# Kernel tuning notes

Hardware: AMD Instinct MI355X
Metric: run time of the kernel (lower is better)

The kernel has to match this reference:

```python
import jax, jax.numpy as jnp
import numpy as np

B, T, C, H = 2, 2048, 1024, 16
HD = C // H  # head dim = 64


def setup_inputs() -> dict:
    key = jax.random.key(0)
    ks = jax.random.split(key, 12)
    s = 1.0 / np.sqrt(C)
    return {
        "q": jax.random.normal(ks[0], (B, T, C), jnp.float32),
        "k": jax.random.normal(ks[1], (B, T, C), jnp.float32),
        "v": jax.random.normal(ks[2], (B, T, C), jnp.float32),
        "attn_bias": jax.random.normal(ks[3], (1, H, T, T), jnp.float32),
        "Wq": jax.random.normal(ks[4], (C, C), jnp.float32) * s,
        "bq": jnp.zeros((C,), jnp.float32),
        "Wk": jax.random.normal(ks[5], (C, C), jnp.float32) * s,
        "bk": jnp.zeros((C,), jnp.float32),
        "Wv": jax.random.normal(ks[6], (C, C), jnp.float32) * s,
        "bv": jnp.zeros((C,), jnp.float32),
        "Wp": jax.random.normal(ks[7], (C, C), jnp.float32) * s,
        "bp": jnp.zeros((C,), jnp.float32),
    }


def reference(q, k, v, attn_bias, Wq, bq, Wk, bk, Wv, bv, Wp, bp):
    # Linear projections (torch Linear: x @ W.T + b), then split heads -> [B,H,T,HD]
    def split_heads(x):
        return x.reshape(B, T, H, HD).transpose(0, 2, 1, 3)

    qh = split_heads(q @ Wq.T + bq)
    kh = split_heads(k @ Wk.T + bk)
    vh = split_heads(v @ Wv.T + bv)

    scale = 1.0 / np.sqrt(HD)
    att = jnp.einsum("bhqd,bhkd->bhqk", qh, kh) * scale  # [B,H,T,T]

    causal = jnp.tril(jnp.ones((T, T), dtype=bool))  # mask[:, :, -Tq:, :Tk]
    att_scores = jnp.where(causal[None, None], att, -jnp.inf)
    att_scores = att_scores + attn_bias

    att_probs = jax.nn.softmax(att_scores, axis=-1)
    y = jnp.einsum("bhqk,bhkd->bhqd", att_probs, vh)
    y = y.transpose(0, 2, 1, 3).reshape(B, T, C)
    y = y @ Wp.T + bp  # dropout p=0.0
    return (y, att_scores)
```

## Files before the change

### kernel.cpp

```cpp
#include <hip/hip_runtime.h>
#include <hip/hip_bf16.h>
#include <math.h>

#define B_ 2
#define T_ 2048
#define C_ 1024
#define H_ 16
#define HD_ 64
#define M_ (B_*T_)
#define K_ 1024

#define SCORE_NINF (-3.0e38f)

#define PART_BH 33792

typedef __attribute__((ext_vector_type(8))) short bf16x8;
typedef __attribute__((ext_vector_type(8))) unsigned short u16x8;
typedef __attribute__((ext_vector_type(4))) float f32x4;

__device__ __forceinline__ ushort f2bf_rne(float x) {
    union { float f; unsigned u; } c; c.f = x;
    unsigned r = c.u + 0x7fffu + ((c.u >> 16) & 1u);
    return (ushort)(r >> 16);
}
__device__ __forceinline__ float bfval(ushort h) {
    union { float f; unsigned u; } c; c.u = ((unsigned)h) << 16; return c.f;
}
__device__ __forceinline__ ushort bf16_hi(float x) {
    union { float f; unsigned u; } c; c.f = x; return (ushort)(c.u >> 16);
}
__device__ __forceinline__ void nt_store_f4(float* p, f32x4 v) {
    __builtin_nontemporal_store(v, (f32x4*)p);
}

__device__ __forceinline__ void gload_lds16(const void* g, void* l) {
    __builtin_amdgcn_global_load_lds(
        (const __attribute__((address_space(1))) unsigned int*)g,
        (__attribute__((address_space(3))) unsigned int*)l, 16, 0, 0);
}

__global__ __launch_bounds__(256) void split_kernel(
    const float* __restrict__ src, ushort* __restrict__ hi,
    ushort* __restrict__ lo, int n)
{
    const int i = (blockIdx.x * 256 + threadIdx.x) * 4;
    if (i >= n) return;
    const float4 x = *(const float4*)&src[i];
    ushort4 h, l;
    h.x = f2bf_rne(x.x); l.x = f2bf_rne(x.x - bfval(h.x));
    h.y = f2bf_rne(x.y); l.y = f2bf_rne(x.y - bfval(h.y));
    h.z = f2bf_rne(x.z); l.z = f2bf_rne(x.z - bfval(h.z));
    h.w = f2bf_rne(x.w); l.w = f2bf_rne(x.w - bfval(h.w));
    *(ushort4*)&hi[i] = h;
    *(ushort4*)&lo[i] = l;
}

template<int MODE, int ASRC>
__global__ __launch_bounds__(256) void gemm_mfma(
    const float*  __restrict__ Xf,
    const ushort* __restrict__ Xh, const ushort* __restrict__ Xl,
    const ushort* __restrict__ Wh, const ushort* __restrict__ Wl,
    const float*  __restrict__ bias,
    float* __restrict__ outf, ushort* __restrict__ out_hi, ushort* __restrict__ out_lo)
{
    constexpr int APITCH = (ASRC == 0) ? 40 : 32;
    __shared__ ushort AhS[128 * APITCH];
    __shared__ ushort AlS[128 * APITCH];
    __shared__ ushort BhS[128 * 32];
    __shared__ ushort BlS[128 * 32];

    const int tid  = threadIdx.x;
    const int lane = tid & 63;
    const int w    = tid >> 6;
    const int lr   = lane & 15, lk = lane >> 4;
    const int wr   = w >> 1,    wc = w & 1;
    const int bm   = blockIdx.x * 128;
    const int bn   = blockIdx.y * 128;

    f32x4 acc[4][4];
    #pragma unroll
    for (int i = 0; i < 4; ++i)
        #pragma unroll
        for (int j = 0; j < 4; ++j) acc[i][j] = (f32x4){0.f, 0.f, 0.f, 0.f};

    const int ar   = tid >> 1;
    const int aseg = (tid & 1) * 16;

    for (int k0 = 0; k0 < K_; k0 += 32) {
        {
            const int r0 = w * 32;
            #pragma unroll
            for (int ii = 0; ii < 2; ++ii) {
                const int rr = r0 + ii * 16;
                const size_t goff = (size_t)(bn + rr + (lane >> 2)) * K_ + k0 + (lane & 3) * 8;
                gload_lds16(Wh + goff, &BhS[rr * 32]);
                gload_lds16(Wl + goff, &BlS[rr * 32]);
            }
            if constexpr (ASRC == 1) {
                #pragma unroll
                for (int ii = 0; ii < 2; ++ii) {
                    const int rr = r0 + ii * 16;
                    const size_t goff = (size_t)(bm + rr + (lane >> 2)) * K_ + k0 + (lane & 3) * 8;
                    gload_lds16(Xh + goff, &AhS[rr * 32]);
                    gload_lds16(Xl + goff, &AlS[rr * 32]);
                }
            }
        }
        if constexpr (ASRC == 0) {
            const float* xp = Xf + (size_t)(bm + ar) * K_ + aseg + k0;
            const float4 f0 = *(const float4*)(xp + 0);
            const float4 f1 = *(const float4*)(xp + 4);
            const float4 f2 = *(const float4*)(xp + 8);
            const float4 f3 = *(const float4*)(xp + 12);
            float xs[16];
            xs[0]=f0.x; xs[1]=f0.y; xs[2]=f0.z; xs[3]=f0.w;
            xs[4]=f1.x; xs[5]=f1.y; xs[6]=f1.z; xs[7]=f1.w;
            xs[8]=f2.x; xs[9]=f2.y; xs[10]=f2.z; xs[11]=f2.w;
            xs[12]=f3.x; xs[13]=f3.y; xs[14]=f3.z; xs[15]=f3.w;
            u16x8 hv[2], lv[2];
            #pragma unroll
            for (int e = 0; e < 16; ++e) {
                const ushort hh = f2bf_rne(xs[e]);
                const ushort ll = f2bf_rne(xs[e] - bfval(hh));
                hv[e >> 3][e & 7] = hh;
                lv[e >> 3][e & 7] = ll;
            }
            *(u16x8*)&AhS[ar * APITCH + aseg]     = hv[0];
            *(u16x8*)&AhS[ar * APITCH + aseg + 8] = hv[1];
            *(u16x8*)&AlS[ar * APITCH + aseg]     = lv[0];
            *(u16x8*)&AlS[ar * APITCH + aseg + 8] = lv[1];
        }
        __syncthreads();

        bf16x8 afr[4][2], bfr[4][2];
        #pragma unroll
        for (int i = 0; i < 4; ++i) {
            const int arow = wr * 64 + i * 16 + lr;
            afr[i][0] = *(const bf16x8*)&AhS[arow * APITCH + lk * 8];
            afr[i][1] = *(const bf16x8*)&AlS[arow * APITCH + lk * 8];
        }
        #pragma unroll
        for (int j = 0; j < 4; ++j) {
            const int brow = wc * 64 + j * 16 + lr;
            bfr[j][0] = *(const bf16x8*)&BhS[brow * 32 + lk * 8];
            bfr[j][1] = *(const bf16x8*)&BlS[brow * 32 + lk * 8];
        }
        #pragma unroll
        for (int i = 0; i < 4; ++i)
            #pragma unroll
            for (int j = 0; j < 4; ++j) {
                acc[i][j] = __builtin_amdgcn_mfma_f32_16x16x32_bf16(afr[i][0], bfr[j][0], acc[i][j], 0, 0, 0);
                acc[i][j] = __builtin_amdgcn_mfma_f32_16x16x32_bf16(afr[i][0], bfr[j][1], acc[i][j], 0, 0, 0);
                acc[i][j] = __builtin_amdgcn_mfma_f32_16x16x32_bf16(afr[i][1], bfr[j][0], acc[i][j], 0, 0, 0);
            }
        __syncthreads();
    }

    const int m0 = bm + wr * 64;
    const int n0 = bn + wc * 64;
    #pragma unroll
    for (int j = 0; j < 4; ++j) {
        const int n = n0 + j * 16 + lr;
        const float bias_n = bias[n];
        #pragma unroll
        for (int i = 0; i < 4; ++i) {
            if constexpr (MODE == 2) {
                const int mbase = m0 + i * 16 + lk * 4;
                const int bb = mbase >> 11, t0 = mbase & 2047;
                const int hh = n >> 6, dd = n & 63;
                ushort4 h4, l4;
                float o;
                o = acc[i][j][0] + bias_n; h4.x = f2bf_rne(o); l4.x = f2bf_rne(o - bfval(h4.x));
                o = acc[i][j][1] + bias_n; h4.y = f2bf_rne(o); l4.y = f2bf_rne(o - bfval(h4.y));
                o = acc[i][j][2] + bias_n; h4.z = f2bf_rne(o); l4.z = f2bf_rne(o - bfval(h4.z));
                o = acc[i][j][3] + bias_n; h4.w = f2bf_rne(o); l4.w = f2bf_rne(o - bfval(h4.w));
                const size_t base = (((size_t)(bb * H_ + hh)) * HD_ + dd) * T_ + t0;
                *(ushort4*)&out_hi[base] = h4;
                *(ushort4*)&out_lo[base] = l4;
            } else {
                #pragma unroll
                for (int q = 0; q < 4; ++q) {
                    const int m = m0 + i * 16 + lk * 4 + q;
                    const float o = acc[i][j][q] + bias_n;
                    if constexpr (MODE == 0) {
                        outf[(size_t)m * C_ + n] = o;
                    } else {
                        const int bb = m >> 11, tt = m & 2047;
                        const int hh = n >> 6, dd = n & 63;
                        const size_t idx = (((size_t)(bb * H_ + hh)) * T_ + tt) * HD_ + dd;
                        const ushort hv2 = f2bf_rne(o);
                        out_hi[idx] = hv2;
                        out_lo[idx] = f2bf_rne(o - bfval(hv2));
                    }
                }
            }
        }
    }
}

__global__ __launch_bounds__(256) void tail_kernel(float* __restrict__ scores)
{
    const int bh = blockIdx.y;
    const int r0 = blockIdx.x * 8;
    const int tid = threadIdx.x;
    const f32x4 ninf4 = (f32x4){SCORE_NINF, SCORE_NINF, SCORE_NINF, SCORE_NINF};
    #pragma unroll
    for (int rr = 0; rr < 8; ++rr) {
        float* row = scores + ((size_t)bh * T_ + r0 + rr) * T_ + 1024;
        nt_store_f4(row + tid * 4, ninf4);
    }
}

#define SPITCH 1028

__global__ __launch_bounds__(256) void score_kernel(
    const ushort* __restrict__ q_hi, const ushort* __restrict__ q_lo,
    const ushort* __restrict__ k_hi, const ushort* __restrict__ k_lo,
    const float* __restrict__ bias,
    float* __restrict__ scores, float2* __restrict__ partials)
{
    __shared__ float tile[16 * SPITCH];

    const int tid  = threadIdx.x;
    const int w    = tid >> 6, lane = tid & 63;
    const int lr   = lane & 15, lk = lane >> 4;

    const int bh = blockIdx.x / 192;
    const int r  = blockIdx.x - bh * 192;
    int s, j;
    if (r < 64) { s = r; j = 0; }
    else        { s = 64 + ((r - 64) >> 1); j = (r - 64) & 1; }
    const int h = bh & 15;
    const int qr0 = s * 16;
    const int cbase = j * 1024;
    const int ktmax = s >> 2;
    const int ktbase = j * 16;

    const ushort* qhb = q_hi + (size_t)bh * T_ * HD_;
    const ushort* qlb = q_lo + (size_t)bh * T_ * HD_;
    const ushort* khb = k_hi + (size_t)bh * T_ * HD_;
    const ushort* klb = k_lo + (size_t)bh * T_ * HD_;

    #pragma unroll
    for (int rr = 0; rr < 4; ++rr) {
        const int row = w * 4 + rr;
        const float* gsrc = bias + ((size_t)h * T_ + qr0 + row) * T_ + cbase + lane * 4;
        #pragma unroll
        for (int ch = 0; ch < 4; ++ch)
            gload_lds16(gsrc + ch * 256, &tile[row * SPITCH + ch * 256]);
    }
    __syncthreads();

    const int qrow = qr0 + lr;
    float2* part_bh = partials + (size_t)bh * PART_BH;
    bf16x8 qf[2][2];
    #pragma unroll
    for (int s2 = 0; s2 < 2; ++s2) {
        const size_t qoff = (size_t)qrow * HD_ + s2 * 32 + lk * 8;
        qf[s2][0] = *(const bf16x8*)&qhb[qoff];
        qf[s2][1] = *(const bf16x8*)&qlb[qoff];
    }
    const f32x4 ninf4 = (f32x4){SCORE_NINF, SCORE_NINF, SCORE_NINF, SCORE_NINF};

    #pragma unroll
    for (int i = 0; i < 4; ++i) {
        const int kt  = ktbase + w * 4 + i;
        const int lc0 = (kt - ktbase) * 64;
        if (kt > ktmax) {
            #pragma unroll
            for (int c = 0; c < 4; ++c)
                *(f32x4*)&tile[lr * SPITCH + lc0 + c * 16 + lk * 4] = ninf4;
            continue;
        }
        const int climit = (kt < ktmax) ? 4 : ((s & 3) + 1);
        f32x4 sc[4];
        #pragma unroll
        for (int c = 0; c < 4; ++c) {
            if (c < climit) {
                f32x4 a = (f32x4){0.f, 0.f, 0.f, 0.f};
                #pragma unroll
                for (int s2 = 0; s2 < 2; ++s2) {
                    const size_t koff = (size_t)(kt * 64 + c * 16 + lr) * HD_ + s2 * 32 + lk * 8;
                    const bf16x8 kfh = *(const bf16x8*)&khb[koff];
                    const bf16x8 kfl = *(const bf16x8*)&klb[koff];
                    a = __builtin_amdgcn_mfma_f32_16x16x32_bf16(kfh, qf[s2][0], a, 0, 0, 0);
                    a = __builtin_amdgcn_mfma_f32_16x16x32_bf16(kfl, qf[s2][0], a, 0, 0, 0);
                    a = __builtin_amdgcn_mfma_f32_16x16x32_bf16(kfh, qf[s2][1], a, 0, 0, 0);
                }
                sc[c] = a;
            }
        }
        float tmax = SCORE_NINF;
        #pragma unroll
        for (int c = 0; c < 4; ++c) {
            const int loff = lr * SPITCH + lc0 + c * 16 + lk * 4;
            if (c < climit) {
                const f32x4 b4 = *(const f32x4*)&tile[loff];
                f32x4 o;
                const int kc0 = kt * 64 + c * 16 + lk * 4;
                #pragma unroll
                for (int q4 = 0; q4 < 4; ++q4) {
                    const float sv = (kc0 + q4 <= qrow) ? sc[c][q4] * 0.125f + b4[q4]
                                                        : SCORE_NINF;
                    sc[c][q4] = sv;
                    tmax = fmaxf(tmax, sv);
                    o[q4] = sv;
                }
                *(f32x4*)&tile[loff] = o;
            } else {
                *(f32x4*)&tile[loff] = ninf4;
            }
        }
        tmax = fmaxf(tmax, __shfl_xor(tmax, 16));
        tmax = fmaxf(tmax, __shfl_xor(tmax, 32));
        float tsum = 0.f;
        #pragma unroll
        for (int c = 0; c < 4; ++c) {
            if (c < climit) {
                tsum += __expf(sc[c][0] - tmax);
                tsum += __expf(sc[c][1] - tmax);
                tsum += __expf(sc[c][2] - tmax);
                tsum += __expf(sc[c][3] - tmax);
            }
        }
        tsum += __shfl_xor(tsum, 16);
        tsum += __shfl_xor(tsum, 32);
        if (lk == 0)
            part_bh[kt * (2080 - 32 * kt) + (qrow - kt * 64)] = make_float2(tmax, tsum);
    }
    __syncthreads();

    #pragma unroll
    for (int row = 0; row < 16; ++row) {
        const f32x4 v = *(const f32x4*)&tile[row * SPITCH + tid * 4];
        *(f32x4*)&scores[((size_t)bh * T_ + qr0 + row) * T_ + cbase + tid * 4] = v;
    }
}

__global__ __launch_bounds__(256) void reduce_kernel(
    const float2* __restrict__ partials, float2* __restrict__ ml)
{
    const int gid = blockIdx.x * 256 + threadIdx.x;
    const int bh = gid >> 11, r = gid & 2047;
    const float2* pb = partials + (size_t)bh * PART_BH;
    const int nt = (r >> 6) + 1;
    float M = SCORE_NINF;
    for (int t = 0; t < nt; ++t)
        M = fmaxf(M, pb[t * (2080 - 32 * t) + (r - (t << 6))].x);
    float L = 0.f;
    for (int t = 0; t < nt; ++t) {
        const float2 p = pb[t * (2080 - 32 * t) + (r - (t << 6))];
        L += p.y * __expf(p.x - M);
    }
    ml[gid] = make_float2(M, 1.f / L);
}

#define PVPITCH 260

__global__ __launch_bounds__(256) void pv_kernel(
    const ushort* __restrict__ vt_hi, const ushort* __restrict__ vt_lo,
    const float* __restrict__ scores, const float2* __restrict__ ml,
    ushort* __restrict__ y_hi, ushort* __restrict__ y_lo)
{
    __shared__ float stile[16 * PVPITCH];

    const int tid = threadIdx.x;
    const int w = tid >> 6, lane = tid & 63;
    const int lr = lane & 15, lk = lane >> 4;
    const int bh = (int)blockIdx.x >> 6;
    const int p  = (int)blockIdx.x & 63;
    const int h = bh & 15, b = bh >> 4;

    const ushort* vhb = vt_hi + (size_t)bh * HD_ * T_;
    const ushort* vlb = vt_lo + (size_t)bh * HD_ * T_;

    #pragma unroll 1
    for (int half = 0; half < 2; ++half) {
        const int s = half ? (127 - p) : p;
        const int qr0 = s * 16;
        const int ktmax = s >> 2;
        const int nch = (ktmax + 4) >> 2;
        const float2 ml2 = ml[(size_t)bh * 2048 + qr0 + lr];
        const float M = ml2.x, invL = ml2.y;

        f32x4 yacc[4];
        #pragma unroll
        for (int c = 0; c < 4; ++c) yacc[c] = (f32x4){0.f, 0.f, 0.f, 0.f};

        #pragma unroll 1
        for (int ch = 0; ch < nch; ++ch) {
            const int cb = ch * 256;
            #pragma unroll
            for (int rr = 0; rr < 4; ++rr) {
                const int row = w * 4 + rr;
                const float* gsrc = scores + ((size_t)bh * T_ + qr0 + row) * T_ + cb + lane * 4;
                gload_lds16(gsrc, &stile[row * PVPITCH]);
            }
            __syncthreads();

            const int kt = ch * 4 + w;
            if (kt <= ktmax) {
                const int climit = (kt < ktmax) ? 4 : ((s & 3) + 1);
                const int s2max = (climit > 2) ? 2 : 1;
                bf16x8 pa[2][2];
                #pragma unroll
                for (int s2 = 0; s2 < 2; ++s2) {
                    if (s2 < s2max) {
                        const float* lsrc = &stile[lr * PVPITCH + w * 64 + s2 * 32 + lk * 8];
                        const f32x4 l0 = *(const f32x4*)(lsrc);
                        const f32x4 l1 = *(const f32x4*)(lsrc + 4);
                        float xs[8];
                        xs[0]=l0[0]; xs[1]=l0[1]; xs[2]=l0[2]; xs[3]=l0[3];
                        xs[4]=l1[0]; xs[5]=l1[1]; xs[6]=l1[2]; xs[7]=l1[3];
                        bf16x8 ph, pl;
                        #pragma unroll
                        for (int jj = 0; jj < 8; ++jj) {
                            const float pv = __expf(xs[jj] - M);
                            const ushort hv = bf16_hi(pv);
                            ph[jj] = (short)hv;
                            pl[jj] = (short)bf16_hi(pv - bfval(hv));
                        }
                        pa[s2][0] = ph;
                        pa[s2][1] = pl;
                    }
                }
                #pragma unroll
                for (int c2 = 0; c2 < 4; ++c2) {
                    #pragma unroll
                    for (int s2 = 0; s2 < 2; ++s2) {
                        if (s2 < s2max) {
                            const size_t voff = (size_t)(c2 * 16 + lr) * T_ + kt * 64 + s2 * 32 + lk * 8;
                            const bf16x8 vfh = *(const bf16x8*)&vhb[voff];
                            const bf16x8 vfl = *(const bf16x8*)&vlb[voff];
                            yacc[c2] = __builtin_amdgcn_mfma_f32_16x16x32_bf16(pa[s2][0], vfh, yacc[c2], 0, 0, 0);
                            yacc[c2] = __builtin_amdgcn_mfma_f32_16x16x32_bf16(pa[s2][0], vfl, yacc[c2], 0, 0, 0);
                            yacc[c2] = __builtin_amdgcn_mfma_f32_16x16x32_bf16(pa[s2][1], vfh, yacc[c2], 0, 0, 0);
                        }
                    }
                }
            }
            __syncthreads();
        }

        float* mbuf = stile;
        if (w > 0) {
            #pragma unroll
            for (int c2 = 0; c2 < 4; ++c2)
                *(f32x4*)&mbuf[((c2 * 3 + (w - 1)) * 64 + lane) * 4] = yacc[c2];
        }
        __syncthreads();
        if (w == 0) {
            float inv[4];
            #pragma unroll
            for (int q4 = 0; q4 < 4; ++q4) inv[q4] = __shfl(invL, lk * 4 + q4);
            #pragma unroll
            for (int c2 = 0; c2 < 4; ++c2) {
                f32x4 tot = yacc[c2];
                #pragma unroll
                for (int ww = 0; ww < 3; ++ww)
                    tot += *(const f32x4*)&mbuf[((c2 * 3 + ww) * 64 + lane) * 4];
                #pragma unroll
                for (int q4 = 0; q4 < 4; ++q4) {
                    const int yr = qr0 + lk * 4 + q4;
                    const float val = tot[q4] * inv[q4];
                    const size_t yi = ((size_t)b * T_ + yr) * C_ + h * HD_ + c2 * 16 + lr;
                    const ushort hv = f2bf_rne(val);
                    y_hi[yi] = hv;
                    y_lo[yi] = f2bf_rne(val - bfval(hv));
                }
            }
        }
        __syncthreads();
    }
}

extern "C" void kernel_launch(void* const* d_in, const int* in_sizes, int n_in,
                              void* d_out, int out_size, void* d_ws, size_t ws_size,
                              hipStream_t stream) {
    const float* q         = (const float*)d_in[0];
    const float* k         = (const float*)d_in[1];
    const float* v         = (const float*)d_in[2];
    const float* attn_bias = (const float*)d_in[3];
    const float* Wq        = (const float*)d_in[4];
    const float* bq        = (const float*)d_in[5];
    const float* Wk        = (const float*)d_in[6];
    const float* bk        = (const float*)d_in[7];
    const float* Wv        = (const float*)d_in[8];
    const float* bv        = (const float*)d_in[9];
    const float* Wp        = (const float*)d_in[10];
    const float* bp        = (const float*)d_in[11];

    float* y_out      = (float*)d_out;
    float* scores_out = y_out + (size_t)B_*T_*C_;

    ushort* ws = (ushort*)d_ws;
    const size_t NE = (size_t)B_*H_*T_*HD_;
    ushort* q_hi  = ws + 0*NE;
    ushort* q_lo  = ws + 1*NE;
    ushort* k_hi  = ws + 2*NE;
    ushort* k_lo  = ws + 3*NE;
    ushort* vt_hi = ws + 4*NE;
    ushort* vt_lo = ws + 5*NE;
    ushort* Wh1   = ws + 6*NE;
    ushort* Wl1   = Wh1 + (size_t)C_*K_;
    float2* partials = (float2*)(ws + 6*NE);
    float2* ml    = (float2*)(ws + 0*NE);
    ushort* y_hi  = ws + 6*NE;
    ushort* y_lo  = ws + 7*NE;
    ushort* Wph   = ws + 2*NE;
    ushort* Wpl   = ws + 3*NE;

    const dim3 gg(M_/128, C_/128);

    split_kernel<<<1024, 256, 0, stream>>>(Wq, Wh1, Wl1, C_*K_);
    gemm_mfma<1,0><<<gg, 256, 0, stream>>>(q, nullptr, nullptr, Wh1, Wl1, bq,
                                           nullptr, q_hi, q_lo);
    split_kernel<<<1024, 256, 0, stream>>>(Wk, Wh1, Wl1, C_*K_);
    gemm_mfma<1,0><<<gg, 256, 0, stream>>>(k, nullptr, nullptr, Wh1, Wl1, bk,
                                           nullptr, k_hi, k_lo);
    split_kernel<<<1024, 256, 0, stream>>>(Wv, Wh1, Wl1, C_*K_);
    gemm_mfma<2,0><<<gg, 256, 0, stream>>>(v, nullptr, nullptr, Wh1, Wl1, bv,
                                           nullptr, vt_hi, vt_lo);

    tail_kernel<<<dim3(128, 32), 256, 0, stream>>>(scores_out);
    score_kernel<<<6144, 256, 0, stream>>>(q_hi, q_lo, k_hi, k_lo, attn_bias,
                                           scores_out, partials);
    reduce_kernel<<<256, 256, 0, stream>>>(partials, ml);
    pv_kernel<<<2048, 256, 0, stream>>>(vt_hi, vt_lo, scores_out, ml, y_hi, y_lo);

    split_kernel<<<1024, 256, 0, stream>>>(Wp, Wph, Wpl, C_*K_);
    gemm_mfma<0,1><<<gg, 256, 0, stream>>>(nullptr, y_hi, y_lo, Wph, Wpl, bp,
                                           y_out, nullptr, nullptr);
}
```

Baseline: 715.2 us.

## Batch weight splits and QKV GEMMs into single launches, fold tail fill into score kernel

Replaces four separate weight hi/lo split launches with one split kernel covering all weights, and merges the three QKV projection GEMMs into one launch using blockIdx.z to select the input. The separate tail kernel that filled the upper half of score rows with -inf is removed, and that fill now happens inside the score kernel. The workspace layout is reshuffled so all split weights coexist, which needs more workspace and carries a risk of buffer aliasing between y, the partials and the q/k buffers.

```diff
diff --git a/kernel.cpp b/kernel.cpp
--- a/kernel.cpp
+++ b/kernel.cpp
@@ -39,12 +39,19 @@
         (__attribute__((address_space(3))) unsigned int*)l, 16, 0, 0);
 }
 
-__global__ __launch_bounds__(256) void split_kernel(
-    const float* __restrict__ src, ushort* __restrict__ hi,
-    ushort* __restrict__ lo, int n)
+__global__ __launch_bounds__(256) void split4_kernel(
+    const float* __restrict__ W0, const float* __restrict__ W1,
+    const float* __restrict__ W2, const float* __restrict__ W3,
+    ushort* __restrict__ h0, ushort* __restrict__ l0,
+    ushort* __restrict__ h1, ushort* __restrict__ l1,
+    ushort* __restrict__ h2, ushort* __restrict__ l2,
+    ushort* __restrict__ h3, ushort* __restrict__ l3)
 {
-    const int i = (blockIdx.x * 256 + threadIdx.x) * 4;
-    if (i >= n) return;
+    const int wsel = blockIdx.x >> 10;
+    const float* src = (wsel == 0) ? W0 : (wsel == 1) ? W1 : (wsel == 2) ? W2 : W3;
+    ushort* hi = (wsel == 0) ? h0 : (wsel == 1) ? h1 : (wsel == 2) ? h2 : h3;
+    ushort* lo = (wsel == 0) ? l0 : (wsel == 1) ? l1 : (wsel == 2) ? l2 : l3;
+    const int i = (((blockIdx.x & 1023) * 256) + threadIdx.x) * 4;
     const float4 x = *(const float4*)&src[i];
     ushort4 h, l;
     h.x = f2bf_rne(x.x); l.x = f2bf_rne(x.x - bfval(h.x));
@@ -55,19 +62,29 @@
     *(ushort4*)&lo[i] = l;
 }
 
-template<int MODE, int ASRC>
-__global__ __launch_bounds__(256) void gemm_mfma(
-    const float*  __restrict__ Xf,
-    const ushort* __restrict__ Xh, const ushort* __restrict__ Xl,
-    const ushort* __restrict__ Wh, const ushort* __restrict__ Wl,
-    const float*  __restrict__ bias,
-    float* __restrict__ outf, ushort* __restrict__ out_hi, ushort* __restrict__ out_lo)
+__global__ __launch_bounds__(256) void gemm_qkv(
+    const float* __restrict__ Xq, const float* __restrict__ Xk, const float* __restrict__ Xv,
+    const ushort* __restrict__ Wqh, const ushort* __restrict__ Wql,
+    const ushort* __restrict__ Wkh, const ushort* __restrict__ Wkl,
+    const ushort* __restrict__ Wvh, const ushort* __restrict__ Wvl,
+    const float* __restrict__ bq, const float* __restrict__ bk, const float* __restrict__ bv,
+    ushort* __restrict__ qo_hi, ushort* __restrict__ qo_lo,
+    ushort* __restrict__ ko_hi, ushort* __restrict__ ko_lo,
+    ushort* __restrict__ vo_hi, ushort* __restrict__ vo_lo)
 {
-    constexpr int APITCH = (ASRC == 0) ? 40 : 32;
+    constexpr int APITCH = 40;
     __shared__ ushort AhS[128 * APITCH];
     __shared__ ushort AlS[128 * APITCH];
     __shared__ ushort BhS[128 * 32];
     __shared__ ushort BlS[128 * 32];
+
+    const int z = blockIdx.z;
+    const float*  Xf = (z == 0) ? Xq : (z == 1) ? Xk : Xv;
+    const ushort* Wh = (z == 0) ? Wqh : (z == 1) ? Wkh : Wvh;
+    const ushort* Wl = (z == 0) ? Wql : (z == 1) ? Wkl : Wvl;
+    const float*  bias = (z == 0) ? bq : (z == 1) ? bk : bv;
+    ushort* out_hi = (z == 0) ? qo_hi : (z == 1) ? ko_hi : vo_hi;
+    ushort* out_lo = (z == 0) ? qo_lo : (z == 1) ? ko_lo : vo_lo;
 
     const int tid  = threadIdx.x;
     const int lane = tid & 63;
@@ -96,17 +113,8 @@
                 gload_lds16(Wh + goff, &BhS[rr * 32]);
                 gload_lds16(Wl + goff, &BlS[rr * 32]);
             }
-            if constexpr (ASRC == 1) {
-                #pragma unroll
-                for (int ii = 0; ii < 2; ++ii) {
-                    const int rr = r0 + ii * 16;
-                    const size_t goff = (size_t)(bm + rr + (lane >> 2)) * K_ + k0 + (lane & 3) * 8;
-                    gload_lds16(Xh + goff, &AhS[rr * 32]);
-                    gload_lds16(Xl + goff, &AlS[rr * 32]);
-                }
-            }
-        }
-        if constexpr (ASRC == 0) {
+        }
+        {
             const float* xp = Xf + (size_t)(bm + ar) * K_ + aseg + k0;
             const float4 f0 = *(const float4*)(xp + 0);
             const float4 f1 = *(const float4*)(xp + 4);
@@ -164,7 +172,7 @@
         const float bias_n = bias[n];
         #pragma unroll
         for (int i = 0; i < 4; ++i) {
-            if constexpr (MODE == 2) {
+            if (z == 2) {
                 const int mbase = m0 + i * 16 + lk * 4;
                 const int bb = mbase >> 11, t0 = mbase & 2047;
                 const int hh = n >> 6, dd = n & 63;
@@ -182,32 +190,91 @@
                 for (int q = 0; q < 4; ++q) {
                     const int m = m0 + i * 16 + lk * 4 + q;
                     const float o = acc[i][j][q] + bias_n;
-                    if constexpr (MODE == 0) {
-                        outf[(size_t)m * C_ + n] = o;
-                    } else {
-                        const int bb = m >> 11, tt = m & 2047;
-                        const int hh = n >> 6, dd = n & 63;
-                        const size_t idx = (((size_t)(bb * H_ + hh)) * T_ + tt) * HD_ + dd;
-                        const ushort hv2 = f2bf_rne(o);
-                        out_hi[idx] = hv2;
-                        out_lo[idx] = f2bf_rne(o - bfval(hv2));
-                    }
+                    const int bb = m >> 11, tt = m & 2047;
+                    const int hh = n >> 6, dd = n & 63;
+                    const size_t idx = (((size_t)(bb * H_ + hh)) * T_ + tt) * HD_ + dd;
+                    const ushort hv2 = f2bf_rne(o);
+                    out_hi[idx] = hv2;
+                    out_lo[idx] = f2bf_rne(o - bfval(hv2));
                 }
             }
         }
     }
 }
 
-__global__ __launch_bounds__(256) void tail_kernel(float* __restrict__ scores)
+__global__ __launch_bounds__(256) void gemm_final(
+    const ushort* __restrict__ Xh, const ushort* __restrict__ Xl,
+    const ushort* __restrict__ Wh, const ushort* __restrict__ Wl,
+    const float*  __restrict__ bias, float* __restrict__ outf)
 {
-    const int bh = blockIdx.y;
-    const int r0 = blockIdx.x * 8;
-    const int tid = threadIdx.x;
-    const f32x4 ninf4 = (f32x4){SCORE_NINF, SCORE_NINF, SCORE_NINF, SCORE_NINF};
-    #pragma unroll
-    for (int rr = 0; rr < 8; ++rr) {
-        float* row = scores + ((size_t)bh * T_ + r0 + rr) * T_ + 1024;
-        nt_store_f4(row + tid * 4, ninf4);
+    __shared__ ushort AhS[128 * 32];
+    __shared__ ushort AlS[128 * 32];
+    __shared__ ushort BhS[128 * 32];
+    __shared__ ushort BlS[128 * 32];
+
+    const int tid  = threadIdx.x;
+    const int lane = tid & 63;
+    const int w    = tid >> 6;
+    const int lr   = lane & 15, lk = lane >> 4;
+    const int wr   = w >> 1,    wc = w & 1;
+    const int bm   = blockIdx.x * 128;
+    const int bn   = blockIdx.y * 128;
+
+    f32x4 acc[4][4];
+    #pragma unroll
+    for (int i = 0; i < 4; ++i)
+        #pragma unroll
+        for (int j = 0; j < 4; ++j) acc[i][j] = (f32x4){0.f, 0.f, 0.f, 0.f};
+
+    for (int k0 = 0; k0 < K_; k0 += 32) {
+        const int r0 = w * 32;
+        #pragma unroll
+        for (int ii = 0; ii < 2; ++ii) {
+            const int rr = r0 + ii * 16;
+            const size_t goffB = (size_t)(bn + rr + (lane >> 2)) * K_ + k0 + (lane & 3) * 8;
+            gload_lds16(Wh + goffB, &BhS[rr * 32]);
+            gload_lds16(Wl + goffB, &BlS[rr * 32]);
+            const size_t goffA = (size_t)(bm + rr + (lane >> 2)) * K_ + k0 + (lane & 3) * 8;
+            gload_lds16(Xh + goffA, &AhS[rr * 32]);
+            gload_lds16(Xl + goffA, &AlS[rr * 32]);
+        }
+        __syncthreads();
+
+        bf16x8 afr[4][2], bfr[4][2];
+        #pragma unroll
+        for (int i = 0; i < 4; ++i) {
+            const int arow = wr * 64 + i * 16 + lr;
+            afr[i][0] = *(const bf16x8*)&AhS[arow * 32 + lk * 8];
+            afr[i][1] = *(const bf16x8*)&AlS[arow * 32 + lk * 8];
+        }
+        #pragma unroll
+        for (int j = 0; j < 4; ++j) {
+            const int brow = wc * 64 + j * 16 + lr;
+            bfr[j][0] = *(const bf16x8*)&BhS[brow * 32 + lk * 8];
+            bfr[j][1] = *(const bf16x8*)&BlS[brow * 32 + lk * 8];
+        }
+        #pragma unroll
+        for (int i = 0; i < 4; ++i)
+            #pragma unroll
+            for (int j = 0; j < 4; ++j) {
+                acc[i][j] = __builtin_amdgcn_mfma_f32_16x16x32_bf16(afr[i][0], bfr[j][0], acc[i][j], 0, 0, 0);
+                acc[i][j] = __builtin_amdgcn_mfma_f32_16x16x32_bf16(afr[i][0], bfr[j][1], acc[i][j], 0, 0, 0);
+                acc[i][j] = __builtin_amdgcn_mfma_f32_16x16x32_bf16(afr[i][1], bfr[j][0], acc[i][j], 0, 0, 0);
+            }
+        __syncthreads();
+    }
+
+    const int m0 = bm + wr * 64;
+    const int n0 = bn + wc * 64;
+    #pragma unroll
+    for (int j = 0; j < 4; ++j) {
+        const int n = n0 + j * 16 + lr;
+        const float bias_n = bias[n];
+        #pragma unroll
+        for (int i = 0; i < 4; ++i)
+            #pragma unroll
+            for (int q = 0; q < 4; ++q)
+                outf[(size_t)(m0 + i * 16 + lk * 4 + q) * C_ + n] = acc[i][j][q] + bias_n;
     }
 }
 
@@ -334,6 +401,12 @@
     for (int row = 0; row < 16; ++row) {
         const f32x4 v = *(const f32x4*)&tile[row * SPITCH + tid * 4];
         *(f32x4*)&scores[((size_t)bh * T_ + qr0 + row) * T_ + cbase + tid * 4] = v;
+    }
+    if (s < 64) {
+        const f32x4 ninf4b = (f32x4){SCORE_NINF, SCORE_NINF, SCORE_NINF, SCORE_NINF};
+        #pragma unroll
+        for (int row = 0; row < 16; ++row)
+            nt_store_f4(&scores[((size_t)bh * T_ + qr0 + row) * T_ + 1024 + tid * 4], ninf4b);
     }
 }
 
@@ -495,40 +568,38 @@
 
     ushort* ws = (ushort*)d_ws;
     const size_t NE = (size_t)B_*H_*T_*HD_;
+    const size_t WN = (size_t)C_*K_;
     ushort* q_hi  = ws + 0*NE;
     ushort* q_lo  = ws + 1*NE;
     ushort* k_hi  = ws + 2*NE;
     ushort* k_lo  = ws + 3*NE;
     ushort* vt_hi = ws + 4*NE;
     ushort* vt_lo = ws + 5*NE;
-    ushort* Wh1   = ws + 6*NE;
-    ushort* Wl1   = Wh1 + (size_t)C_*K_;
-    float2* partials = (float2*)(ws + 6*NE);
+    ushort* Wph   = ws + 6*NE;
+    ushort* Wpl   = Wph + WN;
+    ushort* Wqh   = Wpl + WN;
+    ushort* Wql   = Wqh + WN;
+    ushort* Wkh   = Wql + WN;
+    ushort* Wkl   = Wkh + WN;
+    ushort* Wvh   = Wkl + WN;
+    ushort* Wvl   = Wvh + WN;
+    float2* partials = (float2*)(ws + 6*NE + 2*WN);
     float2* ml    = (float2*)(ws + 0*NE);
-    ushort* y_hi  = ws + 6*NE;
-    ushort* y_lo  = ws + 7*NE;
-    ushort* Wph   = ws + 2*NE;
-    ushort* Wpl   = ws + 3*NE;
-
-    const dim3 gg(M_/128, C_/128);
-
-    split_kernel<<<1024, 256, 0, stream>>>(Wq, Wh1, Wl1, C_*K_);
-    gemm_mfma<1,0><<<gg, 256, 0, stream>>>(q, nullptr, nullptr, Wh1, Wl1, bq,
-                                           nullptr, q_hi, q_lo);
-    split_kernel<<<1024, 256, 0, stream>>>(Wk, Wh1, Wl1, C_*K_);
-    gemm_mfma<1,0><<<gg, 256, 0, stream>>>(k, nullptr, nullptr, Wh1, Wl1, bk,
-                                           nullptr, k_hi, k_lo);
-    split_kernel<<<1024, 256, 0, stream>>>(Wv, Wh1, Wl1, C_*K_);
-    gemm_mfma<2,0><<<gg, 256, 0, stream>>>(v, nullptr, nullptr, Wh1, Wl1, bv,
-                                           nullptr, vt_hi, vt_lo);
-
-    tail_kernel<<<dim3(128, 32), 256, 0, stream>>>(scores_out);
+    ushort* y_hi  = ws + 1*NE;
+    ushort* y_lo  = ws + 2*NE;
+
+    split4_kernel<<<4096, 256, 0, stream>>>(Wq, Wk, Wv, Wp,
+        Wqh, Wql, Wkh, Wkl, Wvh, Wvl, Wph, Wpl);
+
+    gemm_qkv<<<dim3(M_/128, C_/128, 3), 256, 0, stream>>>(
+        q, k, v, Wqh, Wql, Wkh, Wkl, Wvh, Wvl, bq, bk, bv,
+        q_hi, q_lo, k_hi, k_lo, vt_hi, vt_lo);
+
     score_kernel<<<6144, 256, 0, stream>>>(q_hi, q_lo, k_hi, k_lo, attn_bias,
                                            scores_out, partials);
     reduce_kernel<<<256, 256, 0, stream>>>(partials, ml);
     pv_kernel<<<2048, 256, 0, stream>>>(vt_hi, vt_lo, scores_out, ml, y_hi, y_lo);
 
-    split_kernel<<<1024, 256, 0, stream>>>(Wp, Wph, Wpl, C_*K_);
-    gemm_mfma<0,1><<<gg, 256, 0, stream>>>(nullptr, y_hi, y_lo, Wph, Wpl, bp,
-                                           y_out, nullptr, nullptr);
-}
+    gemm_final<<<dim3(M_/128, C_/128), 256, 0, stream>>>(
+        y_hi, y_lo, Wph, Wpl, bp, y_out);
+}
```

Result: faster. 630.7 us (-11.8%).
